# Optimization experiments

Measured on AMD Instinct MI355X. Metric: run time of the kernel, lower is better.

Reference implementation:

```python
import jax, jax.numpy as jnp
import numpy as np

B, S, I, H = 256, 512, 512, 1024


def setup_inputs() -> dict:
    key = jax.random.key(0)
    ks = jax.random.split(key, 7)
    s = 1.0 / np.sqrt(H)
    x = jax.random.normal(ks[0], (B, S, I), jnp.float32)
    # equinox GRUCell params: weight_ih (3H,I), weight_hh (3H,H), bias (3H,), bias_n (H,)
    wi = jax.random.uniform(ks[1], (3 * H, I), jnp.float32, -s, s)
    wh = jax.random.uniform(ks[2], (3 * H, H), jnp.float32, -s, s)
    bi = jax.random.uniform(ks[3], (3 * H,), jnp.float32, -s, s)
    bn = jax.random.uniform(ks[4], (H,), jnp.float32, -s, s)
    # final Linear(H, 1)
    sl = 1.0 / np.sqrt(H)
    wl = jax.random.uniform(ks[5], (1, H), jnp.float32, -sl, sl)
    bl = jax.random.uniform(ks[6], (1,), jnp.float32, -sl, sl)
    return {"x": x, "wi": wi, "wh": wh, "bi": bi, "bn": bn, "wl": wl, "bl": bl}


def reference(x, wi, wh, bi, bn, wl, bl):
    # x: (B, S, I). Precompute input-side gate projections for all timesteps
    # (same math as per-step wi @ x_t + bi, hoisted out of the scan).
    ig_all = jnp.einsum('bsi,gi->sbg', x, wi) + bi  # (S, B, 3H)

    def step(h, ig_t):
        hg = h @ wh.T  # (B, 3H)
        ir, iz, ia = jnp.split(ig_t, 3, axis=-1)
        hr, hz, ha = jnp.split(hg, 3, axis=-1)
        r = jax.nn.sigmoid(ir + hr)          # reset gate
        z = jax.nn.sigmoid(iz + hz)          # update gate (equinox 'inp')
        n = jnp.tanh(ia + r * (ha + bn))     # candidate (uses bias_n)
        h_new = n + z * (h - n)              # equinox GRUCell output
        return h_new, None

    h0 = jnp.zeros((x.shape[0], wh.shape[1]), x.dtype)
    hT, _ = jax.lax.scan(step, h0, ig_all)
    energies = hT @ wl.T + bl  # (B, 1)
    return jnp.squeeze(energies, axis=-1)  # (B,)
```

## Files before the change

### kernel.cpp

```cpp
#include <hip/hip_runtime.h>
#include <hip/hip_bf16.h>


#define B_  256
#define S_  512
#define I_  512
#define H_  1024
#define GSIZE 64

typedef __bf16 bf16x8 __attribute__((ext_vector_type(8)));
typedef float  f32x4  __attribute__((ext_vector_type(4)));

union U16x8 { int4 i; bf16x8 b; unsigned short s[8]; unsigned u[4]; };

__device__ __forceinline__ unsigned pack2bf(float lo, float hi) {
    union { float f; unsigned u; } a, b;
    a.f = lo; b.f = hi;
    return __builtin_amdgcn_perm(b.u + 0x8000u, a.u + 0x8000u, 0x07060302u);
}
__device__ __forceinline__ bf16x8 ldb(const unsigned short* p) {
    U16x8 u; u.i = *(const int4*)p; return u.b;
}
__device__ __forceinline__ bf16x8 ldh_dev(const unsigned long long* p) {
    unsigned long long lo = __hip_atomic_load(p,     __ATOMIC_RELAXED, __HIP_MEMORY_SCOPE_AGENT);
    unsigned long long hi = __hip_atomic_load(p + 1, __ATOMIC_RELAXED, __HIP_MEMORY_SCOPE_AGENT);
    union { unsigned long long q[2]; bf16x8 b; } u;
    u.q[0] = lo; u.q[1] = hi; return u.b;
}

__global__ void prep_kernel(const float* __restrict__ wh, const float* __restrict__ wi,
                            const float* __restrict__ x,
                            unsigned* __restrict__ hbA_u, unsigned* __restrict__ whb_u,
                            unsigned* __restrict__ wib_u, unsigned* __restrict__ flags,
                            unsigned* __restrict__ xb_u) {
    int idx = blockIdx.x * blockDim.x + threadIdx.x;
    int stride = gridDim.x * blockDim.x;
    const float2* wh2 = (const float2*)wh;
    const float2* wi2 = (const float2*)wi;
    for (int i = idx; i < 3 * H_ * H_ / 2; i += stride) { float2 v = wh2[i]; whb_u[i] = pack2bf(v.x, v.y); }
    for (int i = idx; i < 3 * H_ * I_ / 2; i += stride) { float2 v = wi2[i]; wib_u[i] = pack2bf(v.x, v.y); }
    for (int i = idx; i < B_ * H_ / 2; i += stride) hbA_u[i] = 0u;
    if (idx < 256 * 16) flags[idx] = 0u;
    if (xb_u) {
        const float2* x2 = (const float2*)x;
        const int n = B_ * S_ * I_ / 2;
        for (int i = idx; i < n; i += stride) { float2 v = x2[i]; xb_u[i] = pack2bf(v.x, v.y); }
    }
}

template<int XB>
__global__ __launch_bounds__(256, 1) void gru_persistent(
    const float* __restrict__ x,
    const unsigned short* __restrict__ xbp,
    const unsigned short* __restrict__ whb,
    const unsigned short* __restrict__ wib,
    const float* __restrict__ bi,
    const float* __restrict__ bn,
    unsigned short* __restrict__ hbufA,
    unsigned short* __restrict__ hbufB,
    float* __restrict__ h32g,
    unsigned* __restrict__ flags)
{
    __shared__ float partial[4 * 3 * 16 * 68];
    __shared__ float h32s[64 * 17];

    const int tid  = threadIdx.x;
    const int w    = tid >> 6;
    const int lane = tid & 63;
    const int col  = lane & 15;
    const int quad = lane >> 4;

    const int hblk = blockIdx.x & 63;
    const int mt   = blockIdx.x >> 6;
    const int k0   = hblk << 4;
    const int b0   = mt << 6;
    const int kwh  = w << 8;
    const int kwi  = w << 7;

    bf16x8 Bh[3][8];
    bf16x8 Bx[3][4];
    #pragma unroll
    for (int g = 0; g < 3; ++g) {
        const unsigned short* bh = whb + ((size_t)(g * H_ + k0 + col)) * H_ + kwh + (quad << 3);
        #pragma unroll
        for (int kk = 0; kk < 8; ++kk) Bh[g][kk] = ldb(bh + kk * 32);
        const unsigned short* bx = wib + ((size_t)(g * H_ + k0 + col)) * I_ + kwi + (quad << 3);
        #pragma unroll
        for (int kk = 0; kk < 4; ++kk) Bx[g][kk] = ldb(bx + kk * 32);
    }

    const int hcol = k0 + col;
    const float bir = bi[hcol], biz = bi[H_ + hcol], bia = bi[2 * H_ + hcol], bnv = bn[hcol];

    for (int i = tid; i < 64 * 17; i += 256) h32s[i] = 0.f;
    __syncthreads();

    unsigned* myflag = flags + blockIdx.x * 16;
    const unsigned* grpflags = flags + (mt * 64) * 16;

    const f32x4 zero4 = {0.f, 0.f, 0.f, 0.f};

    for (int t = 0; t < S_; ++t) {
        f32x4 acc[4][4];
        #pragma unroll
        for (int mi = 0; mi < 4; ++mi)
            #pragma unroll
            for (int j = 0; j < 4; ++j) acc[mi][j] = zero4;

        if constexpr (XB) {
            const unsigned short* xbase = xbp + ((size_t)(b0 + col) * S_ + (size_t)t) * I_ + kwi + (quad << 3);
            #pragma unroll
            for (int kk = 0; kk < 4; ++kk) {
                #pragma unroll
                for (int mi = 0; mi < 4; ++mi) {
                    bf16x8 a = ldb(xbase + (size_t)mi * 16 * S_ * I_ + kk * 32);
                    acc[mi][0] = __builtin_amdgcn_mfma_f32_16x16x32_bf16(a, Bx[0][kk], acc[mi][0], 0, 0, 0);
                    acc[mi][1] = __builtin_amdgcn_mfma_f32_16x16x32_bf16(a, Bx[1][kk], acc[mi][1], 0, 0, 0);
                    acc[mi][2] = __builtin_amdgcn_mfma_f32_16x16x32_bf16(a, Bx[2][kk], acc[mi][2], 0, 0, 0);
                }
            }
        } else {
            const float* xbase = x + ((size_t)(b0 + col) * S_ + (size_t)t) * I_ + kwi + (quad << 3);
            #pragma unroll
            for (int kk = 0; kk < 4; ++kk) {
                #pragma unroll
                for (int mi = 0; mi < 4; ++mi) {
                    const float* p = xbase + (size_t)mi * 16 * S_ * I_ + kk * 32;
                    float4 f0 = *(const float4*)p;
                    float4 f1 = *(const float4*)(p + 4);
                    U16x8 u;
                    u.u[0] = pack2bf(f0.x, f0.y);
                    u.u[1] = pack2bf(f0.z, f0.w);
                    u.u[2] = pack2bf(f1.x, f1.y);
                    u.u[3] = pack2bf(f1.z, f1.w);
                    bf16x8 a = u.b;
                    acc[mi][0] = __builtin_amdgcn_mfma_f32_16x16x32_bf16(a, Bx[0][kk], acc[mi][0], 0, 0, 0);
                    acc[mi][1] = __builtin_amdgcn_mfma_f32_16x16x32_bf16(a, Bx[1][kk], acc[mi][1], 0, 0, 0);
                    acc[mi][2] = __builtin_amdgcn_mfma_f32_16x16x32_bf16(a, Bx[2][kk], acc[mi][2], 0, 0, 0);
                }
            }
        }

        if (t > 0) {
            if (lane < 16) {
                const unsigned* fp = grpflags + (((w << 4) + lane) << 4);
                while (__hip_atomic_load(fp, __ATOMIC_RELAXED, __HIP_MEMORY_SCOPE_AGENT) < (unsigned)t)
                    __builtin_amdgcn_s_sleep(1);
            }
            asm volatile("" ::: "memory");
        }

        const unsigned short* hcur = (t & 1) ? hbufB : hbufA;
        const unsigned short* hrow = hcur + (size_t)(b0 + col) * H_ + kwh + (quad << 3);
        #pragma unroll
        for (int kk = 0; kk < 8; ++kk) {
            #pragma unroll
            for (int mi = 0; mi < 4; ++mi) {
                bf16x8 a = ldh_dev((const unsigned long long*)(hrow + (size_t)mi * 16 * H_ + kk * 32));
                acc[mi][0] = __builtin_amdgcn_mfma_f32_16x16x32_bf16(a, Bh[0][kk], acc[mi][0], 0, 0, 0);
                acc[mi][1] = __builtin_amdgcn_mfma_f32_16x16x32_bf16(a, Bh[1][kk], acc[mi][1], 0, 0, 0);
                acc[mi][3] = __builtin_amdgcn_mfma_f32_16x16x32_bf16(a, Bh[2][kk], acc[mi][3], 0, 0, 0);
            }
        }

        #pragma unroll
        for (int mi = 0; mi < 4; ++mi) {
            if (mi == w) continue;
            int slot = mi - (mi > w ? 1 : 0);
            float* dst = partial + (size_t)((w * 3 + slot) * 16) * 68;
            #pragma unroll
            for (int j = 0; j < 4; ++j)
                #pragma unroll
                for (int r = 0; r < 4; ++r)
                    dst[((quad << 2) + r) * 68 + j * 16 + col] = acc[mi][j][r];
        }
        __syncthreads();

        #pragma unroll
        for (int r = 0; r < 4; ++r) {
            float sr = 0.f, sz = 0.f, sia = 0.f, sha = 0.f;
            #pragma unroll
            for (int mi = 0; mi < 4; ++mi)
                if (mi == w) { sr = acc[mi][0][r]; sz = acc[mi][1][r]; sia = acc[mi][2][r]; sha = acc[mi][3][r]; }
            #pragma unroll
            for (int p = 0; p < 4; ++p) {
                if (p == w) continue;
                int slot = w - (w > p ? 1 : 0);
                const float* src = partial + (size_t)(((p * 3 + slot) * 16 + (quad << 2) + r)) * 68 + col;
                sr  += src[0];
                sz  += src[16];
                sia += src[32];
                sha += src[48];
            }
            float rg = 1.f / (1.f + __expf(-(sr + bir)));
            float zg = 1.f / (1.f + __expf(-(sz + biz)));
            float pa = sia + bia + rg * (sha + bnv);
            float e2 = __expf(2.f * pa);
            float ng = 1.f - 2.f / (e2 + 1.f);
            int m = (w << 4) + (quad << 2) + r;
            float hold = h32s[m * 17 + col];
            float hnew = ng + zg * (hold - ng);
            h32s[m * 17 + col] = hnew;
            if (t == S_ - 1) h32g[(size_t)(b0 + m) * H_ + k0 + col] = hnew;
        }
        __syncthreads();

        {
            unsigned short* hnext = (t & 1) ? hbufA : hbufB;
            const int m  = tid >> 2;
            const int c4 = (tid & 3) << 2;
            const float* hp = h32s + m * 17 + c4;
            unsigned long long pkt = (unsigned long long)pack2bf(hp[0], hp[1])
                                   | ((unsigned long long)pack2bf(hp[2], hp[3]) << 32);
            __hip_atomic_store((unsigned long long*)(hnext + (size_t)(b0 + m) * H_ + k0 + c4),
                               pkt, __ATOMIC_RELAXED, __HIP_MEMORY_SCOPE_AGENT);
        }
        __syncthreads();

        if (tid == 0)
            __hip_atomic_store(myflag, (unsigned)(t + 1), __ATOMIC_RELAXED, __HIP_MEMORY_SCOPE_AGENT);
    }
}

__global__ __launch_bounds__(256) void final_kernel(const float* __restrict__ h32,
                                                    const float* __restrict__ wl,
                                                    const float* __restrict__ bl,
                                                    float* __restrict__ out) {
    const int b = blockIdx.x;
    float s = 0.f;
    for (int k = threadIdx.x; k < H_; k += 256)
        s += h32[((size_t)b << 10) + k] * wl[k];
    #pragma unroll
    for (int off = 32; off > 0; off >>= 1)
        s += __shfl_down(s, off, 64);
    __shared__ float red[4];
    const int wave = threadIdx.x >> 6;
    const int lane = threadIdx.x & 63;
    if (lane == 0) red[wave] = s;
    __syncthreads();
    if (threadIdx.x == 0)
        out[b] = red[0] + red[1] + red[2] + red[3] + bl[0];
}

extern "C" void kernel_launch(void* const* d_in, const int* in_sizes, int n_in,
                              void* d_out, int out_size, void* d_ws, size_t ws_size,
                              hipStream_t stream) {
    const float* x  = (const float*)d_in[0];
    const float* wi = (const float*)d_in[1];
    const float* wh = (const float*)d_in[2];
    const float* bi = (const float*)d_in[3];
    const float* bn = (const float*)d_in[4];
    const float* wl = (const float*)d_in[5];
    const float* bl = (const float*)d_in[6];
    float* out = (float*)d_out;

    char* ws = (char*)d_ws;
    float*          h32g  = (float*)ws;
    unsigned short* hbA   = (unsigned short*)(ws + (1u << 20));
    unsigned short* hbB   = (unsigned short*)(ws + (1u << 20) + (512u << 10));
    unsigned short* whb   = (unsigned short*)(ws + (2u << 20));
    unsigned short* wib   = (unsigned short*)(ws + (8u << 20));
    unsigned*       flags = (unsigned*)(ws + (11u << 20));
    const bool use_xb = ws_size >= (145ull << 20);
    unsigned short* xbw = use_xb ? (unsigned short*)(ws + (16ull << 20)) : nullptr;

    prep_kernel<<<1024, 256, 0, stream>>>(wh, wi, x, (unsigned*)hbA, (unsigned*)whb,
                                          (unsigned*)wib, flags, (unsigned*)xbw);
    if (use_xb)
        gru_persistent<1><<<256, 256, 0, stream>>>(x, xbw, whb, wib, bi, bn, hbA, hbB, h32g, flags);
    else
        gru_persistent<0><<<256, 256, 0, stream>>>(x, nullptr, whb, wib, bi, bn, hbA, hbB, h32g, flags);
    final_kernel<<<B_, 256, 0, stream>>>(h32g, wl, bl, out);
}
```

Measured before the change: 8.280 ms.

## Use per-wave flags for finer-grained cross-block sync and prefetch h fragments

Replaces the per-block completion flag with one flag per wave, so each wave publishes its slice of h right after its own stores complete (s_waitcnt vmcnt(0)) without a trailing block-wide barrier, and consumers spin on the specific producer waves they depend on using all 64 lanes. The h-operand loads are double-buffered so the next k-slice loads overlap the current MFMAs. Non-temporal loads are used for fp32 x in the fallback path, and the bf16 x workspace offset and threshold move so it is more likely to be enabled. The risks are more flag traffic from spinning lanes and memory-ordering subtleties, since the flag store relies on relaxed atomics after vmcnt.

```diff
diff --git a/kernel.cpp b/kernel.cpp
--- a/kernel.cpp
+++ b/kernel.cpp
@@ -6,10 +6,10 @@
 #define S_  512
 #define I_  512
 #define H_  1024
-#define GSIZE 64
 
 typedef __bf16 bf16x8 __attribute__((ext_vector_type(8)));
 typedef float  f32x4  __attribute__((ext_vector_type(4)));
+typedef float  f32x4v __attribute__((ext_vector_type(4)));
 
 union U16x8 { int4 i; bf16x8 b; unsigned short s[8]; unsigned u[4]; };
 
@@ -40,7 +40,7 @@
     for (int i = idx; i < 3 * H_ * H_ / 2; i += stride) { float2 v = wh2[i]; whb_u[i] = pack2bf(v.x, v.y); }
     for (int i = idx; i < 3 * H_ * I_ / 2; i += stride) { float2 v = wi2[i]; wib_u[i] = pack2bf(v.x, v.y); }
     for (int i = idx; i < B_ * H_ / 2; i += stride) hbA_u[i] = 0u;
-    if (idx < 256 * 16) flags[idx] = 0u;
+    if (idx < 256 * 4 * 16) flags[idx] = 0u;
     if (xb_u) {
         const float2* x2 = (const float2*)x;
         const int n = B_ * S_ * I_ / 2;
@@ -95,8 +95,9 @@
     for (int i = tid; i < 64 * 17; i += 256) h32s[i] = 0.f;
     __syncthreads();
 
-    unsigned* myflag = flags + blockIdx.x * 16;
-    const unsigned* grpflags = flags + (mt * 64) * 16;
+    unsigned* myflag = flags + (((blockIdx.x << 2) + w) << 4);
+    const unsigned* spin_fp = flags +
+        ((((mt << 6) + (w << 4) + (lane >> 2)) * 4 + (lane & 3)) << 4);
 
     const f32x4 zero4 = {0.f, 0.f, 0.f, 0.f};
 
@@ -126,13 +127,13 @@
                 #pragma unroll
                 for (int mi = 0; mi < 4; ++mi) {
                     const float* p = xbase + (size_t)mi * 16 * S_ * I_ + kk * 32;
-                    float4 f0 = *(const float4*)p;
-                    float4 f1 = *(const float4*)(p + 4);
+                    f32x4v f0 = __builtin_nontemporal_load((const f32x4v*)p);
+                    f32x4v f1 = __builtin_nontemporal_load((const f32x4v*)(p + 4));
                     U16x8 u;
-                    u.u[0] = pack2bf(f0.x, f0.y);
-                    u.u[1] = pack2bf(f0.z, f0.w);
-                    u.u[2] = pack2bf(f1.x, f1.y);
-                    u.u[3] = pack2bf(f1.z, f1.w);
+                    u.u[0] = pack2bf(f0[0], f0[1]);
+                    u.u[1] = pack2bf(f0[2], f0[3]);
+                    u.u[2] = pack2bf(f1[0], f1[1]);
+                    u.u[3] = pack2bf(f1[2], f1[3]);
                     bf16x8 a = u.b;
                     acc[mi][0] = __builtin_amdgcn_mfma_f32_16x16x32_bf16(a, Bx[0][kk], acc[mi][0], 0, 0, 0);
                     acc[mi][1] = __builtin_amdgcn_mfma_f32_16x16x32_bf16(a, Bx[1][kk], acc[mi][1], 0, 0, 0);
@@ -142,24 +143,32 @@
         }
 
         if (t > 0) {
-            if (lane < 16) {
-                const unsigned* fp = grpflags + (((w << 4) + lane) << 4);
-                while (__hip_atomic_load(fp, __ATOMIC_RELAXED, __HIP_MEMORY_SCOPE_AGENT) < (unsigned)t)
-                    __builtin_amdgcn_s_sleep(1);
-            }
+            while (__hip_atomic_load(spin_fp, __ATOMIC_RELAXED, __HIP_MEMORY_SCOPE_AGENT) < (unsigned)t)
+                __builtin_amdgcn_s_sleep(1);
             asm volatile("" ::: "memory");
         }
 
         const unsigned short* hcur = (t & 1) ? hbufB : hbufA;
         const unsigned short* hrow = hcur + (size_t)(b0 + col) * H_ + kwh + (quad << 3);
-        #pragma unroll
-        for (int kk = 0; kk < 8; ++kk) {
-            #pragma unroll
-            for (int mi = 0; mi < 4; ++mi) {
-                bf16x8 a = ldh_dev((const unsigned long long*)(hrow + (size_t)mi * 16 * H_ + kk * 32));
-                acc[mi][0] = __builtin_amdgcn_mfma_f32_16x16x32_bf16(a, Bh[0][kk], acc[mi][0], 0, 0, 0);
-                acc[mi][1] = __builtin_amdgcn_mfma_f32_16x16x32_bf16(a, Bh[1][kk], acc[mi][1], 0, 0, 0);
-                acc[mi][3] = __builtin_amdgcn_mfma_f32_16x16x32_bf16(a, Bh[2][kk], acc[mi][3], 0, 0, 0);
+        {
+            bf16x8 hf[2][4];
+            #pragma unroll
+            for (int mi = 0; mi < 4; ++mi)
+                hf[0][mi] = ldh_dev((const unsigned long long*)(hrow + (size_t)mi * 16 * H_));
+            #pragma unroll
+            for (int kk = 0; kk < 8; ++kk) {
+                if (kk < 7) {
+                    #pragma unroll
+                    for (int mi = 0; mi < 4; ++mi)
+                        hf[(kk + 1) & 1][mi] = ldh_dev((const unsigned long long*)(hrow + (size_t)mi * 16 * H_ + (kk + 1) * 32));
+                }
+                #pragma unroll
+                for (int mi = 0; mi < 4; ++mi) {
+                    bf16x8 a = hf[kk & 1][mi];
+                    acc[mi][0] = __builtin_amdgcn_mfma_f32_16x16x32_bf16(a, Bh[0][kk], acc[mi][0], 0, 0, 0);
+                    acc[mi][1] = __builtin_amdgcn_mfma_f32_16x16x32_bf16(a, Bh[1][kk], acc[mi][1], 0, 0, 0);
+                    acc[mi][3] = __builtin_amdgcn_mfma_f32_16x16x32_bf16(a, Bh[2][kk], acc[mi][3], 0, 0, 0);
+                }
             }
         }
 
@@ -207,18 +216,17 @@
 
         {
             unsigned short* hnext = (t & 1) ? hbufA : hbufB;
-            const int m  = tid >> 2;
-            const int c4 = (tid & 3) << 2;
-            const float* hp = h32s + m * 17 + c4;
+            const int pm = (w << 4) + (lane >> 2);
+            const int pc = (lane & 3) << 2;
+            const float* hp = h32s + pm * 17 + pc;
             unsigned long long pkt = (unsigned long long)pack2bf(hp[0], hp[1])
                                    | ((unsigned long long)pack2bf(hp[2], hp[3]) << 32);
-            __hip_atomic_store((unsigned long long*)(hnext + (size_t)(b0 + m) * H_ + k0 + c4),
+            __hip_atomic_store((unsigned long long*)(hnext + (size_t)(b0 + pm) * H_ + k0 + pc),
                                pkt, __ATOMIC_RELAXED, __HIP_MEMORY_SCOPE_AGENT);
-        }
-        __syncthreads();
-
-        if (tid == 0)
-            __hip_atomic_store(myflag, (unsigned)(t + 1), __ATOMIC_RELAXED, __HIP_MEMORY_SCOPE_AGENT);
+            asm volatile("s_waitcnt vmcnt(0)" ::: "memory");
+            if (lane == 0)
+                __hip_atomic_store(myflag, (unsigned)(t + 1), __ATOMIC_RELAXED, __HIP_MEMORY_SCOPE_AGENT);
+        }
     }
 }
 
@@ -261,8 +269,8 @@
     unsigned short* whb   = (unsigned short*)(ws + (2u << 20));
     unsigned short* wib   = (unsigned short*)(ws + (8u << 20));
     unsigned*       flags = (unsigned*)(ws + (11u << 20));
-    const bool use_xb = ws_size >= (145ull << 20);
-    unsigned short* xbw = use_xb ? (unsigned short*)(ws + (16ull << 20)) : nullptr;
+    const bool use_xb = ws_size >= (140ull << 20);
+    unsigned short* xbw = use_xb ? (unsigned short*)(ws + (12ull << 20)) : nullptr;
 
     prep_kernel<<<1024, 256, 0, stream>>>(wh, wi, x, (unsigned*)hbA, (unsigned*)whb,
                                           (unsigned*)wib, flags, (unsigned*)xbw);
```

Result: faster. 7.889 ms (-4.7%).
